# Kernel tuning notes

Hardware: AMD Instinct MI355X
Metric: run time of the kernel (lower is better)

## Reference

```python
import jax, jax.numpy as jnp
import numpy as np

B, N, K, C = 8, 4096, 16, 128
HID, DEPTH = 4 * C, 2
EPS = 1e-5


def _bn(x, g, b, m, v):
    # BatchNorm1d in eval mode over the last (channel) dim
    return (x - m) * (g * jax.lax.rsqrt(v + EPS)) + b


def _ffn(x, w1, b1, w2, b2, g, bt, m, v):
    h = jax.nn.relu(jnp.einsum('bnc,ch->bnh', x, w1) + b1)
    y = jnp.einsum('bnh,hc->bnc', h, w2) + b2
    return _bn(y, g, bt, m, v)


def setup_inputs() -> dict:
    key = jax.random.key(0)
    ks = jax.random.split(key, 24)
    s = 0.05
    inp = {
        'x': jax.random.normal(ks[0], (B, N, C), jnp.float32),
        'knn_idx': jax.random.randint(ks[1], (B, N, K), 0, N, jnp.int64),
        'mlp0_w1': jax.random.normal(ks[2], (C, HID), jnp.float32) * s,
        'mlp0_b1': jax.random.normal(ks[3], (HID,), jnp.float32) * s,
        'mlp0_w2': jax.random.normal(ks[4], (HID, C), jnp.float32) * s,
        'mlp0_b2': jax.random.normal(ks[5], (C,), jnp.float32) * s,
        'mlp0_g': jax.random.uniform(ks[6], (C,), jnp.float32, 0.5, 1.5),
        'mlp0_beta': jax.random.normal(ks[7], (C,), jnp.float32) * s,
        'mlp0_m': jnp.zeros((C,), jnp.float32),
        'mlp0_v': jnp.ones((C,), jnp.float32),
        'vfr_w': jax.random.normal(ks[8], (DEPTH, C, C), jnp.float32) * s,
        'vfr_b': jax.random.normal(ks[9], (DEPTH, C), jnp.float32) * s,
        'vfr_g': jax.random.uniform(ks[10], (DEPTH, C), jnp.float32, 0.5, 1.5),
        'vfr_beta': jax.random.normal(ks[11], (DEPTH, C), jnp.float32) * s,
        'vfr_m': jnp.zeros((DEPTH, C), jnp.float32),
        'vfr_v': jnp.ones((DEPTH, C), jnp.float32),
        'ffn_w1': jax.random.normal(ks[12], (DEPTH, C, HID), jnp.float32) * s,
        'ffn_b1': jax.random.normal(ks[13], (DEPTH, HID), jnp.float32) * s,
        'ffn_w2': jax.random.normal(ks[14], (DEPTH, HID, C), jnp.float32) * s,
        'ffn_b2': jax.random.normal(ks[15], (DEPTH, C), jnp.float32) * s,
        'ffn_g': jax.random.uniform(ks[16], (DEPTH, C), jnp.float32, 0.5, 1.5),
        'ffn_beta': jax.random.normal(ks[17], (DEPTH, C), jnp.float32) * s,
        'ffn_m': jnp.zeros((DEPTH, C), jnp.float32),
        'ffn_v': jnp.ones((DEPTH, C), jnp.float32),
    }
    return inp


def reference(x, knn_idx,
              mlp0_w1, mlp0_b1, mlp0_w2, mlp0_b2, mlp0_g, mlp0_beta, mlp0_m, mlp0_v,
              vfr_w, vfr_b, vfr_g, vfr_beta, vfr_m, vfr_v,
              ffn_w1, ffn_b1, ffn_w2, ffn_b2, ffn_g, ffn_beta, ffn_m, ffn_v):
    # eval mode: DropPath is identity, BatchNorm uses running stats
    x = x + _ffn(x, mlp0_w1, mlp0_b1, mlp0_w2, mlp0_b2, mlp0_g, mlp0_beta, mlp0_m, mlp0_v)
    gather = jax.vmap(lambda pts, idx: pts[idx])  # [N,C],[N,K] -> [N,K,C]
    for i in range(DEPTH):
        # VFR: linear -> knn gather -> edge diff -> max over K -> BN
        h = jnp.einsum('bnc,cd->bnd', x, vfr_w[i]) + vfr_b[i]
        nb = gather(h, knn_idx)                      # [B,N,K,C]
        agg = jnp.max(nb - h[:, :, None, :], axis=2)  # [B,N,C]
        x = x + _bn(agg, vfr_g[i], vfr_beta[i], vfr_m[i], vfr_v[i])
        x = x + _ffn(x, ffn_w1[i], ffn_b1[i], ffn_w2[i], ffn_b2[i],
                     ffn_g[i], ffn_beta[i], ffn_m[i], ffn_v[i])
    return x
```

## Files before the change

kernel.cpp:

```cpp
#include <hip/hip_runtime.h>
#include <hip/hip_bf16.h>
#include <stdint.h>

typedef __attribute__((ext_vector_type(8))) __bf16 bf16x8;
typedef __attribute__((ext_vector_type(4))) float floatx4;

#define EPS 1e-5f

__device__ __forceinline__ unsigned short f2bf(float f) {
    union { float f; unsigned int u; } x; x.f = f;
    unsigned int r = x.u + 0x7fffu + ((x.u >> 16) & 1u);
    return (unsigned short)(r >> 16);
}

__device__ __forceinline__ float bf2f(unsigned int u) {
    union { unsigned int u; float f; } x; x.u = u << 16; return x.f;
}

struct Params {
    const float* x_in;
    const int*   knn;
    const float* w1s[3];
    const float* w2s[3];
    const float* vws[2];
    unsigned short* W1P[3];
    unsigned short* W2P[3];
    unsigned short* VTP[2];
    const float* b1s[3];
    const float* b2s[3];
    const float* gs[3];
    const float* bes[3];
    const float* ms[3];
    const float* vvs[3];
    const float* vbb[2];
    const float* vgg[2];
    const float* vbt[2];
    const float* vmm[2];
    const float* vva[2];
    float* xf;
};

__global__ __launch_bounds__(256) void pack_weights(Params P) {
    const int gtid = blockIdx.x * 256 + threadIdx.x;
    const int GT   = gridDim.x * 256;
#pragma unroll
    for (int t = 0; t < 3; ++t) {
        const float* s1 = P.w1s[t];
        unsigned short* d1 = P.W1P[t];
        for (int idx = gtid; idx < 65536; idx += GT) {
            int h = idx & 511, k = idx >> 9;
            int hf = h >> 7, w = (h >> 4) & 7, ln = h & 15;
            int ks = (k >> 5) & 3, q = (k >> 3) & 3, j = k & 7;
            d1[hf * 16384 + w * 2048 + ks * 512 + q * 128 + ln * 8 + j] = f2bf(s1[idx]);
        }
        const float* s2 = P.w2s[t];
        unsigned short* d2 = P.W2P[t];
        for (int idx = gtid; idx < 65536; idx += GT) {
            int c = idx & 127, h = idx >> 7;
            int hf = h >> 7, ks = (h >> 5) & 3, q = (h >> 3) & 3, j = h & 7;
            int w = c >> 4, ln = c & 15;
            d2[hf * 16384 + w * 2048 + ks * 512 + q * 128 + ln * 8 + j] = f2bf(s2[idx]);
        }
    }
#pragma unroll
    for (int t = 0; t < 2; ++t) {
        const float* sv = P.vws[t];
        unsigned short* dv = P.VTP[t];
        for (int idx = gtid; idx < 16384; idx += GT) {
            int c = idx & 127, k = idx >> 7;
            int ks = (k >> 5) & 3, q = (k >> 3) & 3, j = k & 7;
            int w = c >> 4, ln = c & 15;
            dv[w * 2048 + ks * 512 + q * 128 + ln * 8 + j] = f2bf(sv[idx]);
        }
    }
}

template <int LOADX, int TE, int TF, int TV>
__global__ __launch_bounds__(512, 4)
void stage(Params P, const float* __restrict__ xold_g,
           const unsigned short* __restrict__ VbIn,
           unsigned short* __restrict__ VbOut)
{
    __shared__ __align__(16) unsigned short xt[8192];
    __shared__ __align__(16) float xf32[8192];
    __shared__ __align__(16) uint2 ht2[2][2048];
    const int tid  = threadIdx.x;
    const int lane = tid & 63;
    const int w    = tid >> 6;
    const int q    = lane >> 4;
    const int ln   = lane & 15;
    const int sw   = ln & 7;
    const int phys = blockIdx.x;
    const int bid  = (phys & 7) * 64 + (phys >> 3);
    const int p0   = bid << 6;
    const floatx4 zero = {0.f, 0.f, 0.f, 0.f};

    if constexpr (LOADX) {
        const int r = tid >> 3, seg = tid & 7;
        const float4* src = (const float4*)(xold_g + (size_t)(p0 + r) * 128 + seg * 16);
        float4* dstf = (float4*)&xf32[r * 128 + seg * 16];
#pragma unroll
        for (int i = 0; i < 2; ++i) {
            float4 a = src[2 * i];
            float4 b = src[2 * i + 1];
            dstf[2 * i]     = a;
            dstf[2 * i + 1] = b;
            int kq = seg * 2 + i;
            uint4 pk;
            pk.x = (unsigned int)f2bf(a.x) | ((unsigned int)f2bf(a.y) << 16);
            pk.y = (unsigned int)f2bf(a.z) | ((unsigned int)f2bf(a.w) << 16);
            pk.z = (unsigned int)f2bf(b.x) | ((unsigned int)f2bf(b.y) << 16);
            pk.w = (unsigned int)f2bf(b.z) | ((unsigned int)f2bf(b.w) << 16);
            *(uint4*)&xt[(r * 16 + (kq ^ (r & 7))) * 8] = pk;
        }
    }

    if constexpr (TE >= 0) {
        const int c0 = lane << 1;
        float2 gv = *(const float2*)(P.vgg[TE] + c0);
        float2 bv = *(const float2*)(P.vbt[TE] + c0);
        float2 mv = *(const float2*)(P.vmm[TE] + c0);
        float2 vv = *(const float2*)(P.vva[TE] + c0);
        const float sc0 = gv.x * rsqrtf(vv.x + EPS);
        const float sc1 = gv.y * rsqrtf(vv.y + EPS);
#pragma unroll
        for (int it = 0; it < 8; ++it) {
            const int pl = it * 8 + w;
            const int p  = p0 + pl;
            const int b  = p >> 12;
            const size_t rowoff = (size_t)p * 128 + c0;
            unsigned int su = *(const unsigned int*)(VbIn + rowoff);
            const int4* kp4 = (const int4*)(P.knn + (size_t)p * 16);
            int4 ka = kp4[0], kb = kp4[1], kc = kp4[2], kd = kp4[3];
            const unsigned short* vbase = VbIn + (((size_t)b << 12) << 7) + c0;
            float m0 = -3.4e38f, m1 = -3.4e38f;
            unsigned int u;
#define GATH(IDX) u = *(const unsigned int*)(vbase + ((size_t)(IDX) << 7)); \
            m0 = fmaxf(m0, bf2f(u & 0xffffu)); m1 = fmaxf(m1, bf2f(u >> 16));
            GATH(ka.x) GATH(ka.y) GATH(ka.z) GATH(ka.w)
            GATH(kb.x) GATH(kb.y) GATH(kb.z) GATH(kb.w)
            GATH(kc.x) GATH(kc.y) GATH(kc.z) GATH(kc.w)
            GATH(kd.x) GATH(kd.y) GATH(kd.z) GATH(kd.w)
#undef GATH
            float s0 = bf2f(su & 0xffffu), s1 = bf2f(su >> 16);
            float y0 = (m0 - s0 - mv.x) * sc0 + bv.x;
            float y1 = (m1 - s1 - mv.y) * sc1 + bv.y;
            float2 xv = *(const float2*)(xold_g + rowoff);
            float xn0 = xv.x + y0, xn1 = xv.y + y1;
            *(float2*)&xf32[pl * 128 + c0] = make_float2(xn0, xn1);
            unsigned int pk = (unsigned int)f2bf(xn0) | ((unsigned int)f2bf(xn1) << 16);
            ((unsigned int*)xt)[(pl * 16 + ((lane >> 2) ^ (pl & 7))) * 4 + (lane & 3)] = pk;
        }
    }
    __syncthreads();

    floatx4 acc2[4];
#pragma unroll
    for (int i = 0; i < 4; ++i) acc2[i] = zero;

    const unsigned short* W1 = P.W1P[TF];
    const unsigned short* W2 = P.W2P[TF];
    const float* b1 = P.b1s[TF];

#pragma unroll
    for (int hf2 = 0; hf2 < 2; ++hf2) {
#pragma unroll
        for (int hh = 0; hh < 2; ++hh) {
            const int hf = 2 * hf2 + hh;
            floatx4 acc1[4];
#pragma unroll
            for (int i = 0; i < 4; ++i) acc1[i] = zero;
            const unsigned short* a1 = W1 + hf * 16384 + w * 2048 + q * 128 + ln * 8;
            __builtin_amdgcn_s_setprio(1);
#pragma unroll
            for (int ks = 0; ks < 4; ++ks) {
                bf16x8 af = *(const bf16x8*)(a1 + ks * 512);
#pragma unroll
                for (int nt = 0; nt < 4; ++nt) {
                    bf16x8 bfr = *(const bf16x8*)&xt[((16 * nt + ln) * 16 + ((4 * ks + q) ^ sw)) * 8];
                    acc1[nt] = __builtin_amdgcn_mfma_f32_16x16x32_bf16(af, bfr, acc1[nt], 0, 0, 0);
                }
            }
            __builtin_amdgcn_s_setprio(0);
            {
                const int hid0 = 16 * w + 4 * q;
                const int ghid = 128 * hf + hid0;
                const float bv0 = b1[ghid + 0], bv1 = b1[ghid + 1];
                const float bv2 = b1[ghid + 2], bv3 = b1[ghid + 3];
                const int c16  = hid0 >> 3;
                const int half = q & 1;
#pragma unroll
                for (int nt = 0; nt < 4; ++nt) {
                    const int pt = 16 * nt + ln;
                    float v0 = acc1[nt][0] + bv0; v0 = v0 > 0.f ? v0 : 0.f;
                    float v1 = acc1[nt][1] + bv1; v1 = v1 > 0.f ? v1 : 0.f;
                    float v2 = acc1[nt][2] + bv2; v2 = v2 > 0.f ? v2 : 0.f;
                    float v3 = acc1[nt][3] + bv3; v3 = v3 > 0.f ? v3 : 0.f;
                    uint2 pk;
                    pk.x = (unsigned int)f2bf(v0) | ((unsigned int)f2bf(v1) << 16);
                    pk.y = (unsigned int)f2bf(v2) | ((unsigned int)f2bf(v3) << 16);
                    ht2[hh][(pt * 16 + (c16 ^ (pt & 7))) * 2 + half] = pk;
                }
            }
        }
        __syncthreads();
        __builtin_amdgcn_s_setprio(1);
#pragma unroll
        for (int hh = 0; hh < 2; ++hh) {
            const int hf = 2 * hf2 + hh;
            const unsigned short* b2b = W2 + hf * 16384 + w * 2048 + q * 128 + ln * 8;
#pragma unroll
            for (int ks = 0; ks < 4; ++ks) {
                bf16x8 bw = *(const bf16x8*)(b2b + ks * 512);
#pragma unroll
                for (int mt = 0; mt < 4; ++mt) {
                    bf16x8 ah = *(const bf16x8*)&ht2[hh][((16 * mt + ln) * 16 + ((4 * ks + q) ^ sw)) * 2];
                    acc2[mt] = __builtin_amdgcn_mfma_f32_16x16x32_bf16(ah, bw, acc2[mt], 0, 0, 0);
                }
            }
        }
        __builtin_amdgcn_s_setprio(0);
        if (hf2 == 0) __syncthreads();
    }

    {
        const float* b2   = P.b2s[TF];
        const float* gam  = P.gs[TF];
        const float* bet  = P.bes[TF];
        const float* mean = P.ms[TF];
        const float* var  = P.vvs[TF];
        const int c = 16 * w + ln;
        const float bia = b2[c];
        const float sc  = gam[c] * rsqrtf(var[c] + EPS);
        const float bb  = bet[c];
        const float mu  = mean[c];
#pragma unroll
        for (int mt = 0; mt < 4; ++mt) {
#pragma unroll
            for (int r = 0; r < 4; ++r) {
                const int rl = 16 * mt + 4 * q + r;
                float v  = acc2[mt][r] + bia;
                float y  = (v - mu) * sc + bb;
                float xn = xf32[rl * 128 + c] + y;
                P.xf[(size_t)(p0 + rl) * 128 + c] = xn;
                if constexpr (TV >= 0)
                    xt[(rl * 16 + ((c >> 3) ^ (rl & 7))) * 8 + (c & 7)] = f2bf(xn);
            }
        }
    }

    if constexpr (TV >= 0) {
        __syncthreads();
        const unsigned short* VT = P.VTP[TV];
        const float* vb = P.vbb[TV];
        floatx4 acc[4];
#pragma unroll
        for (int i = 0; i < 4; ++i) acc[i] = zero;
        const unsigned short* bb2 = VT + w * 2048 + q * 128 + ln * 8;
        __builtin_amdgcn_s_setprio(1);
#pragma unroll
        for (int ks = 0; ks < 4; ++ks) {
            bf16x8 bw = *(const bf16x8*)(bb2 + ks * 512);
#pragma unroll
            for (int mt = 0; mt < 4; ++mt) {
                bf16x8 ax = *(const bf16x8*)&xt[((16 * mt + ln) * 16 + ((4 * ks + q) ^ sw)) * 8];
                acc[mt] = __builtin_amdgcn_mfma_f32_16x16x32_bf16(ax, bw, acc[mt], 0, 0, 0);
            }
        }
        __builtin_amdgcn_s_setprio(0);
        const int c = 16 * w + ln;
        const float bia = vb[c];
#pragma unroll
        for (int mt = 0; mt < 4; ++mt)
#pragma unroll
            for (int r = 0; r < 4; ++r)
                VbOut[(size_t)(p0 + 16 * mt + 4 * q + r) * 128 + c] = f2bf(acc[mt][r] + bia);
    }
}

extern "C" void kernel_launch(void* const* d_in, const int* in_sizes, int n_in,
                              void* d_out, int out_size, void* d_ws, size_t ws_size,
                              hipStream_t stream)
{
    Params p;
    p.x_in = (const float*)d_in[0];
    p.knn  = (const int*)d_in[1];
    const float* w1  = (const float*)d_in[2];
    const float* b1  = (const float*)d_in[3];
    const float* w2  = (const float*)d_in[4];
    const float* b2  = (const float*)d_in[5];
    const float* g0  = (const float*)d_in[6];
    const float* be0 = (const float*)d_in[7];
    const float* m0p = (const float*)d_in[8];
    const float* v0p = (const float*)d_in[9];
    const float* vw  = (const float*)d_in[10];
    const float* vbp = (const float*)d_in[11];
    const float* vgp = (const float*)d_in[12];
    const float* vbe = (const float*)d_in[13];
    const float* vmp = (const float*)d_in[14];
    const float* vvp = (const float*)d_in[15];
    const float* fw1 = (const float*)d_in[16];
    const float* fb1 = (const float*)d_in[17];
    const float* fw2 = (const float*)d_in[18];
    const float* fb2 = (const float*)d_in[19];
    const float* fg  = (const float*)d_in[20];
    const float* fbe = (const float*)d_in[21];
    const float* fm  = (const float*)d_in[22];
    const float* fv  = (const float*)d_in[23];

    p.w1s[0] = w1;  p.w1s[1] = fw1; p.w1s[2] = fw1 + 65536;
    p.w2s[0] = w2;  p.w2s[1] = fw2; p.w2s[2] = fw2 + 65536;
    p.vws[0] = vw;  p.vws[1] = vw + 16384;
    p.b1s[0] = b1;  p.b1s[1] = fb1; p.b1s[2] = fb1 + 512;
    p.b2s[0] = b2;  p.b2s[1] = fb2; p.b2s[2] = fb2 + 128;
    p.gs[0]  = g0;  p.gs[1]  = fg;  p.gs[2]  = fg + 128;
    p.bes[0] = be0; p.bes[1] = fbe; p.bes[2] = fbe + 128;
    p.ms[0]  = m0p; p.ms[1]  = fm;  p.ms[2]  = fm + 128;
    p.vvs[0] = v0p; p.vvs[1] = fv;  p.vvs[2] = fv + 128;
    p.vbb[0] = vbp; p.vbb[1] = vbp + 128;
    p.vgg[0] = vgp; p.vgg[1] = vgp + 128;
    p.vbt[0] = vbe; p.vbt[1] = vbe + 128;
    p.vmm[0] = vmp; p.vmm[1] = vmp + 128;
    p.vva[0] = vvp; p.vva[1] = vvp + 128;

    char* ws = (char*)d_ws;
    unsigned short* Vb0 = (unsigned short*)ws;
    unsigned short* Vb1 = (unsigned short*)(ws + (size_t)(8 << 20));
    unsigned short* u   = (unsigned short*)(ws + (size_t)(16 << 20));
    for (int i = 0; i < 3; ++i) p.W1P[i] = u + i * 65536;
    for (int i = 0; i < 3; ++i) p.W2P[i] = u + 196608 + i * 65536;
    for (int i = 0; i < 2; ++i) p.VTP[i] = u + 393216 + i * 16384;
    p.xf = (float*)d_out;

    pack_weights<<<dim3(512), 256, 0, stream>>>(p);
    stage<1, -1, 0, 0><<<dim3(512), 512, 0, stream>>>(p, p.x_in, nullptr, Vb0);
    stage<0,  0, 1, 1><<<dim3(512), 512, 0, stream>>>(p, p.xf, Vb0, Vb1);
    stage<0,  1, 2, -1><<<dim3(512), 512, 0, stream>>>(p, p.xf, Vb1, nullptr);
}
```

Measured before the change: 185.4 us.

## Fuse three stage kernels into one persistent kernel with per-batch spin barriers

Merges the three stage launches into a single kernel that keeps each block's x tile in shared memory across all layers. Blocks synchronise per batch through atomic counters and spin-wait before the kNN gather, which removes kernel launch gaps and the fp32 x round-trips through global memory. The weight-pack kernel is rewritten so each thread emits one vectorised 16-byte packed store and also zeroes the counters. The spin barrier assumes all 512 blocks are co-resident and has a bounded spin that could silently proceed if they are not.

```diff
diff --git a/kernel.cpp b/kernel.cpp
--- a/kernel.cpp
+++ b/kernel.cpp
@@ -17,7 +17,7 @@
     union { unsigned int u; float f; } x; x.u = u << 16; return x.f;
 }
 
-struct Params {
+struct Params2 {
     const float* x_in;
     const int*   knn;
     const float* w1s[3];
@@ -37,49 +37,66 @@
     const float* vbt[2];
     const float* vmm[2];
     const float* vva[2];
+    unsigned short* Vb0;
+    unsigned short* Vb1;
+    unsigned int*   ctr;
     float* xf;
 };
 
-__global__ __launch_bounds__(256) void pack_weights(Params P) {
+__global__ __launch_bounds__(256) void pack2(Params2 P) {
     const int gtid = blockIdx.x * 256 + threadIdx.x;
-    const int GT   = gridDim.x * 256;
-#pragma unroll
-    for (int t = 0; t < 3; ++t) {
+    unsigned short v[8];
+    if (gtid < 24576) {
+        const int t = gtid >> 13;
+        const int d = (gtid & 8191) << 3;
+        const int hf = d >> 14, w = (d >> 11) & 7, ks = (d >> 9) & 3,
+                  q = (d >> 7) & 3, ln = (d >> 3) & 15;
         const float* s1 = P.w1s[t];
-        unsigned short* d1 = P.W1P[t];
-        for (int idx = gtid; idx < 65536; idx += GT) {
-            int h = idx & 511, k = idx >> 9;
-            int hf = h >> 7, w = (h >> 4) & 7, ln = h & 15;
-            int ks = (k >> 5) & 3, q = (k >> 3) & 3, j = k & 7;
-            d1[hf * 16384 + w * 2048 + ks * 512 + q * 128 + ln * 8 + j] = f2bf(s1[idx]);
-        }
+        const int hcol = 128 * hf + 16 * w + ln;
+        const int kb   = 32 * ks + 8 * q;
+#pragma unroll
+        for (int j = 0; j < 8; ++j) v[j] = f2bf(s1[(kb + j) * 512 + hcol]);
+        uint4 pk;
+        pk.x = v[0] | ((unsigned)v[1] << 16); pk.y = v[2] | ((unsigned)v[3] << 16);
+        pk.z = v[4] | ((unsigned)v[5] << 16); pk.w = v[6] | ((unsigned)v[7] << 16);
+        *(uint4*)&P.W1P[t][d] = pk;
+    } else if (gtid < 49152) {
+        const int g = gtid - 24576;
+        const int t = g >> 13;
+        const int d = (g & 8191) << 3;
+        const int hf = d >> 14, w = (d >> 11) & 7, ks = (d >> 9) & 3,
+                  q = (d >> 7) & 3, ln = (d >> 3) & 15;
         const float* s2 = P.w2s[t];
-        unsigned short* d2 = P.W2P[t];
-        for (int idx = gtid; idx < 65536; idx += GT) {
-            int c = idx & 127, h = idx >> 7;
-            int hf = h >> 7, ks = (h >> 5) & 3, q = (h >> 3) & 3, j = h & 7;
-            int w = c >> 4, ln = c & 15;
-            d2[hf * 16384 + w * 2048 + ks * 512 + q * 128 + ln * 8 + j] = f2bf(s2[idx]);
-        }
+        const int col = 16 * w + ln;
+        const int hb  = 128 * hf + 32 * ks + 8 * q;
+#pragma unroll
+        for (int j = 0; j < 8; ++j) v[j] = f2bf(s2[(hb + j) * 128 + col]);
+        uint4 pk;
+        pk.x = v[0] | ((unsigned)v[1] << 16); pk.y = v[2] | ((unsigned)v[3] << 16);
+        pk.z = v[4] | ((unsigned)v[5] << 16); pk.w = v[6] | ((unsigned)v[7] << 16);
+        *(uint4*)&P.W2P[t][d] = pk;
+    } else if (gtid < 53248) {
+        const int g = gtid - 49152;
+        const int t = g >> 11;
+        const int d = (g & 2047) << 3;
+        const int w = (d >> 11) & 7, ks = (d >> 9) & 3,
+                  q = (d >> 7) & 3, ln = (d >> 3) & 15;
+        const float* sv = P.vws[t];
+        const int col = 16 * w + ln;
+        const int kb  = 32 * ks + 8 * q;
+#pragma unroll
+        for (int j = 0; j < 8; ++j) v[j] = f2bf(sv[(kb + j) * 128 + col]);
+        uint4 pk;
+        pk.x = v[0] | ((unsigned)v[1] << 16); pk.y = v[2] | ((unsigned)v[3] << 16);
+        pk.z = v[4] | ((unsigned)v[5] << 16); pk.w = v[6] | ((unsigned)v[7] << 16);
+        *(uint4*)&P.VTP[t][d] = pk;
+    } else if (gtid < 53264) {
+        P.ctr[gtid - 53248] = 0;
     }
-#pragma unroll
-    for (int t = 0; t < 2; ++t) {
-        const float* sv = P.vws[t];
-        unsigned short* dv = P.VTP[t];
-        for (int idx = gtid; idx < 16384; idx += GT) {
-            int c = idx & 127, k = idx >> 7;
-            int ks = (k >> 5) & 3, q = (k >> 3) & 3, j = k & 7;
-            int w = c >> 4, ln = c & 15;
-            dv[w * 2048 + ks * 512 + q * 128 + ln * 8 + j] = f2bf(sv[idx]);
-        }
-    }
-}
-
-template <int LOADX, int TE, int TF, int TV>
+}
+
 __global__ __launch_bounds__(512, 4)
-void stage(Params P, const float* __restrict__ xold_g,
-           const unsigned short* __restrict__ VbIn,
-           unsigned short* __restrict__ VbOut)
+void fused(Params2 P)
 {
     __shared__ __align__(16) unsigned short xt[8192];
     __shared__ __align__(16) float xf32[8192];
@@ -93,11 +110,12 @@
     const int phys = blockIdx.x;
     const int bid  = (phys & 7) * 64 + (phys >> 3);
     const int p0   = bid << 6;
+    const int batch = phys & 7;
     const floatx4 zero = {0.f, 0.f, 0.f, 0.f};
 
-    if constexpr (LOADX) {
+    {
         const int r = tid >> 3, seg = tid & 7;
-        const float4* src = (const float4*)(xold_g + (size_t)(p0 + r) * 128 + seg * 16);
+        const float4* src = (const float4*)(P.x_in + (size_t)(p0 + r) * 128 + seg * 16);
         float4* dstf = (float4*)&xf32[r * 128 + seg * 16];
 #pragma unroll
         for (int i = 0; i < 2; ++i) {
@@ -114,15 +132,139 @@
             *(uint4*)&xt[(r * 16 + (kq ^ (r & 7))) * 8] = pk;
         }
     }
-
-    if constexpr (TE >= 0) {
+    __syncthreads();
+
+    auto ffn_body = [&](int tf, bool final_out) {
+        floatx4 acc2[4];
+#pragma unroll
+        for (int i = 0; i < 4; ++i) acc2[i] = zero;
+        const unsigned short* W1 = P.W1P[tf];
+        const unsigned short* W2 = P.W2P[tf];
+        const float* b1 = P.b1s[tf];
+#pragma unroll
+        for (int hf2 = 0; hf2 < 2; ++hf2) {
+#pragma unroll
+            for (int hh = 0; hh < 2; ++hh) {
+                const int hf = 2 * hf2 + hh;
+                floatx4 acc1[4];
+#pragma unroll
+                for (int i = 0; i < 4; ++i) acc1[i] = zero;
+                const unsigned short* a1 = W1 + hf * 16384 + w * 2048 + q * 128 + ln * 8;
+                __builtin_amdgcn_s_setprio(1);
+#pragma unroll
+                for (int ks = 0; ks < 4; ++ks) {
+                    bf16x8 af = *(const bf16x8*)(a1 + ks * 512);
+#pragma unroll
+                    for (int nt = 0; nt < 4; ++nt) {
+                        bf16x8 bfr = *(const bf16x8*)&xt[((16 * nt + ln) * 16 + ((4 * ks + q) ^ sw)) * 8];
+                        acc1[nt] = __builtin_amdgcn_mfma_f32_16x16x32_bf16(af, bfr, acc1[nt], 0, 0, 0);
+                    }
+                }
+                __builtin_amdgcn_s_setprio(0);
+                {
+                    const int hid0 = 16 * w + 4 * q;
+                    const int ghid = 128 * hf + hid0;
+                    const float bv0 = b1[ghid + 0], bv1 = b1[ghid + 1];
+                    const float bv2 = b1[ghid + 2], bv3 = b1[ghid + 3];
+                    const int c16  = hid0 >> 3;
+                    const int half = q & 1;
+#pragma unroll
+                    for (int nt = 0; nt < 4; ++nt) {
+                        const int pt = 16 * nt + ln;
+                        float v0 = acc1[nt][0] + bv0; v0 = v0 > 0.f ? v0 : 0.f;
+                        float v1 = acc1[nt][1] + bv1; v1 = v1 > 0.f ? v1 : 0.f;
+                        float v2 = acc1[nt][2] + bv2; v2 = v2 > 0.f ? v2 : 0.f;
+                        float v3 = acc1[nt][3] + bv3; v3 = v3 > 0.f ? v3 : 0.f;
+                        uint2 pk;
+                        pk.x = (unsigned int)f2bf(v0) | ((unsigned int)f2bf(v1) << 16);
+                        pk.y = (unsigned int)f2bf(v2) | ((unsigned int)f2bf(v3) << 16);
+                        ht2[hh][(pt * 16 + (c16 ^ (pt & 7))) * 2 + half] = pk;
+                    }
+                }
+            }
+            __syncthreads();
+            __builtin_amdgcn_s_setprio(1);
+#pragma unroll
+            for (int hh = 0; hh < 2; ++hh) {
+                const int hf = 2 * hf2 + hh;
+                const unsigned short* b2b = W2 + hf * 16384 + w * 2048 + q * 128 + ln * 8;
+#pragma unroll
+                for (int ks = 0; ks < 4; ++ks) {
+                    bf16x8 bw = *(const bf16x8*)(b2b + ks * 512);
+#pragma unroll
+                    for (int mt = 0; mt < 4; ++mt) {
+                        bf16x8 ah = *(const bf16x8*)&ht2[hh][((16 * mt + ln) * 16 + ((4 * ks + q) ^ sw)) * 2];
+                        acc2[mt] = __builtin_amdgcn_mfma_f32_16x16x32_bf16(ah, bw, acc2[mt], 0, 0, 0);
+                    }
+                }
+            }
+            __builtin_amdgcn_s_setprio(0);
+            if (hf2 == 0) __syncthreads();
+        }
+        const float* b2   = P.b2s[tf];
+        const float* gam  = P.gs[tf];
+        const float* bet  = P.bes[tf];
+        const float* mean = P.ms[tf];
+        const float* var  = P.vvs[tf];
+        const int c = 16 * w + ln;
+        const float bia = b2[c];
+        const float sc  = gam[c] * rsqrtf(var[c] + EPS);
+        const float bb  = bet[c];
+        const float mu  = mean[c];
+#pragma unroll
+        for (int mt = 0; mt < 4; ++mt) {
+#pragma unroll
+            for (int r = 0; r < 4; ++r) {
+                const int rl = 16 * mt + 4 * q + r;
+                float vv = acc2[mt][r] + bia;
+                float y  = (vv - mu) * sc + bb;
+                float xn = xf32[rl * 128 + c] + y;
+                if (final_out) {
+                    P.xf[(size_t)(p0 + rl) * 128 + c] = xn;
+                } else {
+                    xf32[rl * 128 + c] = xn;
+                    xt[(rl * 16 + ((c >> 3) ^ (rl & 7))) * 8 + (c & 7)] = f2bf(xn);
+                }
+            }
+        }
+    };
+
+    auto vfr_body = [&](int tv, unsigned short* VbOut) {
+        __syncthreads();
+        const unsigned short* VT = P.VTP[tv];
+        const float* vb = P.vbb[tv];
+        floatx4 acc[4];
+#pragma unroll
+        for (int i = 0; i < 4; ++i) acc[i] = zero;
+        const unsigned short* bb2 = VT + w * 2048 + q * 128 + ln * 8;
+        __builtin_amdgcn_s_setprio(1);
+#pragma unroll
+        for (int ks = 0; ks < 4; ++ks) {
+            bf16x8 bw = *(const bf16x8*)(bb2 + ks * 512);
+#pragma unroll
+            for (int mt = 0; mt < 4; ++mt) {
+                bf16x8 ax = *(const bf16x8*)&xt[((16 * mt + ln) * 16 + ((4 * ks + q) ^ sw)) * 8];
+                acc[mt] = __builtin_amdgcn_mfma_f32_16x16x32_bf16(ax, bw, acc[mt], 0, 0, 0);
+            }
+        }
+        __builtin_amdgcn_s_setprio(0);
+        const int c = 16 * w + ln;
+        const float bia = vb[c];
+#pragma unroll
+        for (int mt = 0; mt < 4; ++mt)
+#pragma unroll
+            for (int r = 0; r < 4; ++r)
+                VbOut[(size_t)(p0 + 16 * mt + 4 * q + r) * 128 + c] = f2bf(acc[mt][r] + bia);
+    };
+
+    auto te_body = [&](int te, const unsigned short* VbIn) {
         const int c0 = lane << 1;
-        float2 gv = *(const float2*)(P.vgg[TE] + c0);
-        float2 bv = *(const float2*)(P.vbt[TE] + c0);
-        float2 mv = *(const float2*)(P.vmm[TE] + c0);
-        float2 vv = *(const float2*)(P.vva[TE] + c0);
-        const float sc0 = gv.x * rsqrtf(vv.x + EPS);
-        const float sc1 = gv.y * rsqrtf(vv.y + EPS);
+        float2 gv = *(const float2*)(P.vgg[te] + c0);
+        float2 bv = *(const float2*)(P.vbt[te] + c0);
+        float2 mv = *(const float2*)(P.vmm[te] + c0);
+        float2 vvv = *(const float2*)(P.vva[te] + c0);
+        const float sc0 = gv.x * rsqrtf(vvv.x + EPS);
+        const float sc1 = gv.y * rsqrtf(vvv.y + EPS);
 #pragma unroll
         for (int it = 0; it < 8; ++it) {
             const int pl = it * 8 + w;
@@ -145,144 +287,48 @@
             float s0 = bf2f(su & 0xffffu), s1 = bf2f(su >> 16);
             float y0 = (m0 - s0 - mv.x) * sc0 + bv.x;
             float y1 = (m1 - s1 - mv.y) * sc1 + bv.y;
-            float2 xv = *(const float2*)(xold_g + rowoff);
+            float2 xv = *(const float2*)&xf32[pl * 128 + c0];
             float xn0 = xv.x + y0, xn1 = xv.y + y1;
             *(float2*)&xf32[pl * 128 + c0] = make_float2(xn0, xn1);
             unsigned int pk = (unsigned int)f2bf(xn0) | ((unsigned int)f2bf(xn1) << 16);
             ((unsigned int*)xt)[(pl * 16 + ((lane >> 2) ^ (pl & 7))) * 4 + (lane & 3)] = pk;
         }
-    }
+    };
+
+    auto bbar = [&](unsigned int target) {
+        __syncthreads();
+        if (tid == 0) {
+            __hip_atomic_fetch_add(&P.ctr[batch], 1u, __ATOMIC_RELEASE,
+                                   __HIP_MEMORY_SCOPE_AGENT);
+            unsigned int spins = 0;
+            while (__hip_atomic_load(&P.ctr[batch], __ATOMIC_ACQUIRE,
+                                     __HIP_MEMORY_SCOPE_AGENT) < target
+                   && spins < 2000000u) {
+                ++spins;
+                __builtin_amdgcn_s_sleep(8);
+            }
+        }
+        __syncthreads();
+    };
+
+    ffn_body(0, false);
+    vfr_body(0, P.Vb0);
+    bbar(64);
+    te_body(0, P.Vb0);
     __syncthreads();
-
-    floatx4 acc2[4];
-#pragma unroll
-    for (int i = 0; i < 4; ++i) acc2[i] = zero;
-
-    const unsigned short* W1 = P.W1P[TF];
-    const unsigned short* W2 = P.W2P[TF];
-    const float* b1 = P.b1s[TF];
-
-#pragma unroll
-    for (int hf2 = 0; hf2 < 2; ++hf2) {
-#pragma unroll
-        for (int hh = 0; hh < 2; ++hh) {
-            const int hf = 2 * hf2 + hh;
-            floatx4 acc1[4];
-#pragma unroll
-            for (int i = 0; i < 4; ++i) acc1[i] = zero;
-            const unsigned short* a1 = W1 + hf * 16384 + w * 2048 + q * 128 + ln * 8;
-            __builtin_amdgcn_s_setprio(1);
-#pragma unroll
-            for (int ks = 0; ks < 4; ++ks) {
-                bf16x8 af = *(const bf16x8*)(a1 + ks * 512);
-#pragma unroll
-                for (int nt = 0; nt < 4; ++nt) {
-                    bf16x8 bfr = *(const bf16x8*)&xt[((16 * nt + ln) * 16 + ((4 * ks + q) ^ sw)) * 8];
-                    acc1[nt] = __builtin_amdgcn_mfma_f32_16x16x32_bf16(af, bfr, acc1[nt], 0, 0, 0);
-                }
-            }
-            __builtin_amdgcn_s_setprio(0);
-            {
-                const int hid0 = 16 * w + 4 * q;
-                const int ghid = 128 * hf + hid0;
-                const float bv0 = b1[ghid + 0], bv1 = b1[ghid + 1];
-                const float bv2 = b1[ghid + 2], bv3 = b1[ghid + 3];
-                const int c16  = hid0 >> 3;
-                const int half = q & 1;
-#pragma unroll
-                for (int nt = 0; nt < 4; ++nt) {
-                    const int pt = 16 * nt + ln;
-                    float v0 = acc1[nt][0] + bv0; v0 = v0 > 0.f ? v0 : 0.f;
-                    float v1 = acc1[nt][1] + bv1; v1 = v1 > 0.f ? v1 : 0.f;
-                    float v2 = acc1[nt][2] + bv2; v2 = v2 > 0.f ? v2 : 0.f;
-                    float v3 = acc1[nt][3] + bv3; v3 = v3 > 0.f ? v3 : 0.f;
-                    uint2 pk;
-                    pk.x = (unsigned int)f2bf(v0) | ((unsigned int)f2bf(v1) << 16);
-                    pk.y = (unsigned int)f2bf(v2) | ((unsigned int)f2bf(v3) << 16);
-                    ht2[hh][(pt * 16 + (c16 ^ (pt & 7))) * 2 + half] = pk;
-                }
-            }
-        }
-        __syncthreads();
-        __builtin_amdgcn_s_setprio(1);
-#pragma unroll
-        for (int hh = 0; hh < 2; ++hh) {
-            const int hf = 2 * hf2 + hh;
-            const unsigned short* b2b = W2 + hf * 16384 + w * 2048 + q * 128 + ln * 8;
-#pragma unroll
-            for (int ks = 0; ks < 4; ++ks) {
-                bf16x8 bw = *(const bf16x8*)(b2b + ks * 512);
-#pragma unroll
-                for (int mt = 0; mt < 4; ++mt) {
-                    bf16x8 ah = *(const bf16x8*)&ht2[hh][((16 * mt + ln) * 16 + ((4 * ks + q) ^ sw)) * 2];
-                    acc2[mt] = __builtin_amdgcn_mfma_f32_16x16x32_bf16(ah, bw, acc2[mt], 0, 0, 0);
-                }
-            }
-        }
-        __builtin_amdgcn_s_setprio(0);
-        if (hf2 == 0) __syncthreads();
-    }
-
-    {
-        const float* b2   = P.b2s[TF];
-        const float* gam  = P.gs[TF];
-        const float* bet  = P.bes[TF];
-        const float* mean = P.ms[TF];
-        const float* var  = P.vvs[TF];
-        const int c = 16 * w + ln;
-        const float bia = b2[c];
-        const float sc  = gam[c] * rsqrtf(var[c] + EPS);
-        const float bb  = bet[c];
-        const float mu  = mean[c];
-#pragma unroll
-        for (int mt = 0; mt < 4; ++mt) {
-#pragma unroll
-            for (int r = 0; r < 4; ++r) {
-                const int rl = 16 * mt + 4 * q + r;
-                float v  = acc2[mt][r] + bia;
-                float y  = (v - mu) * sc + bb;
-                float xn = xf32[rl * 128 + c] + y;
-                P.xf[(size_t)(p0 + rl) * 128 + c] = xn;
-                if constexpr (TV >= 0)
-                    xt[(rl * 16 + ((c >> 3) ^ (rl & 7))) * 8 + (c & 7)] = f2bf(xn);
-            }
-        }
-    }
-
-    if constexpr (TV >= 0) {
-        __syncthreads();
-        const unsigned short* VT = P.VTP[TV];
-        const float* vb = P.vbb[TV];
-        floatx4 acc[4];
-#pragma unroll
-        for (int i = 0; i < 4; ++i) acc[i] = zero;
-        const unsigned short* bb2 = VT + w * 2048 + q * 128 + ln * 8;
-        __builtin_amdgcn_s_setprio(1);
-#pragma unroll
-        for (int ks = 0; ks < 4; ++ks) {
-            bf16x8 bw = *(const bf16x8*)(bb2 + ks * 512);
-#pragma unroll
-            for (int mt = 0; mt < 4; ++mt) {
-                bf16x8 ax = *(const bf16x8*)&xt[((16 * mt + ln) * 16 + ((4 * ks + q) ^ sw)) * 8];
-                acc[mt] = __builtin_amdgcn_mfma_f32_16x16x32_bf16(ax, bw, acc[mt], 0, 0, 0);
-            }
-        }
-        __builtin_amdgcn_s_setprio(0);
-        const int c = 16 * w + ln;
-        const float bia = vb[c];
-#pragma unroll
-        for (int mt = 0; mt < 4; ++mt)
-#pragma unroll
-            for (int r = 0; r < 4; ++r)
-                VbOut[(size_t)(p0 + 16 * mt + 4 * q + r) * 128 + c] = f2bf(acc[mt][r] + bia);
-    }
+    ffn_body(1, false);
+    vfr_body(1, P.Vb1);
+    bbar(128);
+    te_body(1, P.Vb1);
+    __syncthreads();
+    ffn_body(2, true);
 }
 
 extern "C" void kernel_launch(void* const* d_in, const int* in_sizes, int n_in,
                               void* d_out, int out_size, void* d_ws, size_t ws_size,
                               hipStream_t stream)
 {
-    Params p;
+    Params2 p;
     p.x_in = (const float*)d_in[0];
     p.knn  = (const int*)d_in[1];
     const float* w1  = (const float*)d_in[2];
@@ -324,16 +370,15 @@
     p.vva[0] = vvp; p.vva[1] = vvp + 128;
 
     char* ws = (char*)d_ws;
-    unsigned short* Vb0 = (unsigned short*)ws;
-    unsigned short* Vb1 = (unsigned short*)(ws + (size_t)(8 << 20));
-    unsigned short* u   = (unsigned short*)(ws + (size_t)(16 << 20));
+    p.Vb0 = (unsigned short*)ws;
+    p.Vb1 = (unsigned short*)(ws + (size_t)(8 << 20));
+    unsigned short* u = (unsigned short*)(ws + (size_t)(16 << 20));
     for (int i = 0; i < 3; ++i) p.W1P[i] = u + i * 65536;
     for (int i = 0; i < 3; ++i) p.W2P[i] = u + 196608 + i * 65536;
     for (int i = 0; i < 2; ++i) p.VTP[i] = u + 393216 + i * 16384;
-    p.xf = (float*)d_out;
-
-    pack_weights<<<dim3(512), 256, 0, stream>>>(p);
-    stage<1, -1, 0, 0><<<dim3(512), 512, 0, stream>>>(p, p.x_in, nullptr, Vb0);
-    stage<0,  0, 1, 1><<<dim3(512), 512, 0, stream>>>(p, p.xf, Vb0, Vb1);
-    stage<0,  1, 2, -1><<<dim3(512), 512, 0, stream>>>(p, p.xf, Vb1, nullptr);
-}
+    p.ctr = (unsigned int*)(ws + (size_t)(17 << 20));
+    p.xf  = (float*)d_out;
+
+    pack2<<<dim3(209), 256, 0, stream>>>(p);
+    fused<<<dim3(512), dim3(512), 0, stream>>>(p);
+}
```

Measured after the change: 427.8 us. +130.7%, slower.
